# Performance work log

Hardware: AMD Instinct MI355X
Metric: run time of the kernel (lower is better)

Reference implementation:

```python
import jax, jax.numpy as jnp
import numpy as np


def _dense_image_warp(image, flow):
    """Faithful JAX port of tfa.image.dense_image_warp.

    image: [B,H,W,C] float, flow: [B,H,W,2] float (flow[...,0]=dy, flow[...,1]=dx).
    query point (y,x) = grid(y,x) - flow; bilinear interp with TFA's clamping:
    floor clipped to [0, size-2], alpha clipped to [0,1].
    """
    B, H, W, C = image.shape
    gy, gx = jnp.meshgrid(
        jnp.arange(H, dtype=flow.dtype), jnp.arange(W, dtype=flow.dtype), indexing="ij"
    )
    qy = gy[None] - flow[..., 0]  # [B,H,W]
    qx = gx[None] - flow[..., 1]

    y0f = jnp.clip(jnp.floor(qy), 0.0, H - 2)
    x0f = jnp.clip(jnp.floor(qx), 0.0, W - 2)
    ay = jnp.clip(qy - y0f, 0.0, 1.0)[..., None]  # [B,H,W,1]
    ax = jnp.clip(qx - x0f, 0.0, 1.0)[..., None]

    y0 = y0f.astype(jnp.int32)
    x0 = x0f.astype(jnp.int32)
    b = jnp.arange(B, dtype=jnp.int32)[:, None, None]

    tl = image[b, y0, x0]          # top-left  [B,H,W,C]
    tr = image[b, y0, x0 + 1]      # top-right
    bl = image[b, y0 + 1, x0]      # bottom-left
    br = image[b, y0 + 1, x0 + 1]  # bottom-right

    top = tl + ax * (tr - tl)
    bot = bl + ax * (br - bl)
    return top + ay * (bot - top)


def setup_inputs() -> dict:
    key = jax.random.key(0)
    k1, k2 = jax.random.split(key)
    B, H, W, C = 8, 1024, 768, 3
    image = jax.random.normal(k1, (B, H, W, C), dtype=jnp.float32)
    # flow magnitudes of a few pixels, typical for appearance-flow warping
    flow = jax.random.normal(k2, (B, H, W, 2), dtype=jnp.float32) * 5.0
    return {"image": image, "flow": flow}


def reference(image, flow):
    return _dense_image_warp(image, flow)
```

## Files before the change

kernel.cpp:

```cpp
#include <hip/hip_runtime.h>


constexpr int B = 8;
constexpr int H = 1024;
constexpr int W = 768;
constexpr int C = 3;

constexpr int TY = 32;
constexpr int TX = 24;
constexpr int TILES_Y = H / TY;
constexpr int COLS_X  = W / TX;

constexpr int WIN_COLS = 64;
constexpr int WSF = WIN_COLS * C;
constexpr int ROW_CHUNKS = WSF / 4;
constexpr int BAND = TY;
constexpr int RING_ROWS = 4 * BAND;
constexpr int BAND_GROUPS = BAND * ROW_CHUNKS / 64;
constexpr int NTHREADS = TY * TX;
constexpr int NWAVES = NTHREADS / 64;
constexpr int GPW = BAND_GROUPS / NWAVES;

static_assert(GPW * NWAVES == BAND_GROUPS, "uniform staging required for vmcnt");

typedef float vfloat2 __attribute__((ext_vector_type(2)));
typedef float vfloat4 __attribute__((ext_vector_type(4)));
typedef float vfloat2_a4 __attribute__((ext_vector_type(2), aligned(4)));
typedef float vfloat4_a4 __attribute__((ext_vector_type(4), aligned(4)));

__global__ __launch_bounds__(NTHREADS) void warp_kernel(
    const float* __restrict__ image,
    const float* __restrict__ flow,
    float* __restrict__ out)
{
    __shared__ float win[RING_ROWS * WSF];

    const int b  = blockIdx.x & 7;
    const int tx = blockIdx.x >> 3;
    const int X0 = tx * TX;
    const int colLo = min(max(X0 - 20, 0), W - WIN_COLS);

    const int lane = threadIdx.x & 63;
    const int wv   = threadIdx.x >> 6;

    const int py  = threadIdx.x / TX;
    const int pxx = threadIdx.x - py * TX;
    const int xg  = X0 + pxx;
    const float xgf = (float)xg;

    const float* gcol = image + (size_t)b * H * (W * C) + colLo * C;

    auto stage_band = [&](int k) {
        const int slotBase = (k & 3) * BAND;
#pragma unroll
        for (int i = 0; i < GPW; ++i) {
            const int j  = i * NWAVES + wv;
            const int ci = j * 64 + lane;
            const int r  = ci / ROW_CHUNKS;
            const int c  = ci - r * ROW_CHUNKS;
            const int rimg = min(k * BAND + r, H - 1);
            const float* g = gcol + (size_t)rimg * (W * C) + c * 4;
            __builtin_amdgcn_global_load_lds(
                (const __attribute__((address_space(1))) void*)g,
                (__attribute__((address_space(3))) void*)(win + slotBase * WSF + j * 256),
                16, 0, 0);
        }
    };

    auto load_flow = [&](int t) -> vfloat2 {
        const int yf = min(t * TY + py, H - 1);
        return __builtin_nontemporal_load(
            (const vfloat2*)flow + (((size_t)b * H + yf) * W + xg));
    };

    stage_band(0);
    stage_band(1);
    vfloat2 fcur = load_flow(0);

#pragma unroll 1
    for (int t = 0; t < TILES_Y; ++t) {
        stage_band(t + 2);
        const vfloat2 fnxt = load_flow(t + 1);

        asm volatile("s_waitcnt vmcnt(3)" ::: "memory");
        __builtin_amdgcn_s_barrier();
        __builtin_amdgcn_sched_barrier(0);

        const int Y0 = t * TY;
        const int y  = Y0 + py;

        const float qy = (float)y - fcur.x;
        const float qx = xgf      - fcur.y;

        float y0f = floorf(qy);
        float x0f = floorf(qx);
        y0f = fminf(fmaxf(y0f, 0.0f), (float)(H - 2));
        x0f = fminf(fmaxf(x0f, 0.0f), (float)(W - 2));
        const float ay = fminf(fmaxf(qy - y0f, 0.0f), 1.0f);
        const float ax = fminf(fmaxf(qx - x0f, 0.0f), 1.0f);
        const int y0 = (int)y0f;
        const int x0 = (int)x0f;

        float tl0, tl1, tl2, tr0, tr1, tr2, bl0, bl1, bl2, br0, br1, br2;

        const bool inwin = (y0 >= Y0 - BAND) & (y0 <= Y0 + 2 * BAND - 2) &
                           (x0 >= colLo) & (x0 <= colLo + WIN_COLS - 2);
        if (inwin) {
            const float* tp = &win[(y0 & (RING_ROWS - 1)) * WSF + (x0 - colLo) * C];
            const float* bp = &win[((y0 + 1) & (RING_ROWS - 1)) * WSF + (x0 - colLo) * C];
            tl0 = tp[0]; tl1 = tp[1]; tl2 = tp[2];
            tr0 = tp[3]; tr1 = tp[4]; tr2 = tp[5];
            bl0 = bp[0]; bl1 = bp[1]; bl2 = bp[2];
            br0 = bp[3]; br1 = bp[4]; br2 = bp[5];
        } else {
            const float* top = image + (((size_t)b * H + y0) * W + x0) * C;
            const float* bot = top + (size_t)W * C;
            const vfloat4 t4 = *(const vfloat4_a4*)top;
            const vfloat2 t2 = *(const vfloat2_a4*)(top + 4);
            const vfloat4 b4 = *(const vfloat4_a4*)bot;
            const vfloat2 b2 = *(const vfloat2_a4*)(bot + 4);
            tl0 = t4.x; tl1 = t4.y; tl2 = t4.z;
            tr0 = t4.w; tr1 = t2.x; tr2 = t2.y;
            bl0 = b4.x; bl1 = b4.y; bl2 = b4.z;
            br0 = b4.w; br1 = b2.x; br2 = b2.y;
        }

        const float tp0 = tl0 + ax * (tr0 - tl0);
        const float tp1 = tl1 + ax * (tr1 - tl1);
        const float tp2 = tl2 + ax * (tr2 - tl2);
        const float bo0 = bl0 + ax * (br0 - bl0);
        const float bo1 = bl1 + ax * (br1 - bl1);
        const float bo2 = bl2 + ax * (br2 - bl2);

        float* o = out + (((size_t)b * H + y) * W + xg) * C;
        __builtin_nontemporal_store(tp0 + ay * (bo0 - tp0), &o[0]);
        __builtin_nontemporal_store(tp1 + ay * (bo1 - tp1), &o[1]);
        __builtin_nontemporal_store(tp2 + ay * (bo2 - tp2), &o[2]);

        __builtin_amdgcn_s_barrier();
        __builtin_amdgcn_sched_barrier(0);
        fcur = fnxt;
    }
}

extern "C" void kernel_launch(void* const* d_in, const int* in_sizes, int n_in,
                              void* d_out, int out_size, void* d_ws, size_t ws_size,
                              hipStream_t stream) {
    const float* image = (const float*)d_in[0];
    const float* flow  = (const float*)d_in[1];
    float* out = (float*)d_out;

    dim3 grid(B * COLS_X);
    dim3 block(NTHREADS);
    warp_kernel<<<grid, block, 0, stream>>>(image, flow, out);
}
```

Baseline: 192.1 us.

## Sweep tiles along x with a panel ring buffer instead of along y

The kernel changes from blocks that own a column strip and walk down the rows to blocks that own a 16-row strip and walk across x in 32-pixel tiles. Each step stages a 49-row by 32-column panel into a four-slot LDS ring holding 128 columns. This cuts the per-block window footprint and makes flow loads and output stores contiguous along rows. The grid grows from 256 to 512 blocks of 512 threads with an occupancy hint of 4 blocks. The cost is a larger halo in y (49 rows staged for 16 output rows), which raises redundant image traffic through LDS, and a deeper vmcnt wait.

```diff
diff --git a/kernel.cpp b/kernel.cpp
--- a/kernel.cpp
+++ b/kernel.cpp
@@ -6,91 +6,94 @@
 constexpr int W = 768;
 constexpr int C = 3;
 
-constexpr int TY = 32;
-constexpr int TX = 24;
-constexpr int TILES_Y = H / TY;
-constexpr int COLS_X  = W / TX;
+constexpr int TY = 16, TX = 32;
+constexpr int TILES_X = W / TX;
+constexpr int STRIPS  = H / TY;
+constexpr int WIN_ROWS = 49;
+constexpr int ROW_CHUNKS = TX * C / 4;
+constexpr int PANEL_CHUNKS = WIN_ROWS * ROW_CHUNKS;
+constexpr int SLOT_FLOATS = PANEL_CHUNKS * 4;
+constexpr int LAST_BASE = PANEL_CHUNKS - 64;
 
-constexpr int WIN_COLS = 64;
-constexpr int WSF = WIN_COLS * C;
-constexpr int ROW_CHUNKS = WSF / 4;
-constexpr int BAND = TY;
-constexpr int RING_ROWS = 4 * BAND;
-constexpr int BAND_GROUPS = BAND * ROW_CHUNKS / 64;
 constexpr int NTHREADS = TY * TX;
 constexpr int NWAVES = NTHREADS / 64;
-constexpr int GPW = BAND_GROUPS / NWAVES;
-
-static_assert(GPW * NWAVES == BAND_GROUPS, "uniform staging required for vmcnt");
+constexpr int IPW = 3;
 
 typedef float vfloat2 __attribute__((ext_vector_type(2)));
 typedef float vfloat4 __attribute__((ext_vector_type(4)));
 typedef float vfloat2_a4 __attribute__((ext_vector_type(2), aligned(4)));
 typedef float vfloat4_a4 __attribute__((ext_vector_type(4), aligned(4)));
 
-__global__ __launch_bounds__(NTHREADS) void warp_kernel(
+__global__ __launch_bounds__(NTHREADS, 4) void warp_kernel(
     const float* __restrict__ image,
     const float* __restrict__ flow,
     float* __restrict__ out)
 {
-    __shared__ float win[RING_ROWS * WSF];
+    __shared__ float win[4 * SLOT_FLOATS];
 
     const int b  = blockIdx.x & 7;
-    const int tx = blockIdx.x >> 3;
-    const int X0 = tx * TX;
-    const int colLo = min(max(X0 - 20, 0), W - WIN_COLS);
+    const int gy = blockIdx.x >> 3;
+    const int Y0 = gy * TY;
+    const int rowLo = min(max(Y0 - 16, 0), H - WIN_ROWS);
 
     const int lane = threadIdx.x & 63;
     const int wv   = threadIdx.x >> 6;
 
-    const int py  = threadIdx.x / TX;
-    const int pxx = threadIdx.x - py * TX;
-    const int xg  = X0 + pxx;
-    const float xgf = (float)xg;
+    const int py  = threadIdx.x >> 5;
+    const int pxx = threadIdx.x & 31;
+    const int y   = Y0 + py;
+    const float yf = (float)y;
+    const size_t rowBase = ((size_t)b * H + y) * W;
 
-    const float* gcol = image + (size_t)b * H * (W * C) + colLo * C;
+    const float* gstrip = image + ((size_t)b * H + rowLo) * (W * C);
 
-    auto stage_band = [&](int k) {
-        const int slotBase = (k & 3) * BAND;
+    auto stage_panel = [&](int p) {
+        const int pe = min(max(p, 0), TILES_X - 1);
+        const float* gp = gstrip + pe * TX * C;
+        float* lp = win + (p & 3) * SLOT_FLOATS;
 #pragma unroll
-        for (int i = 0; i < GPW; ++i) {
-            const int j  = i * NWAVES + wv;
-            const int ci = j * 64 + lane;
-            const int r  = ci / ROW_CHUNKS;
-            const int c  = ci - r * ROW_CHUNKS;
-            const int rimg = min(k * BAND + r, H - 1);
-            const float* g = gcol + (size_t)rimg * (W * C) + c * 4;
+        for (int i = 0; i < IPW; ++i) {
+            const int j   = i * NWAVES + wv;
+            const int off = (j * 64 <= LAST_BASE) ? j * 64 : LAST_BASE;
+            const int ci  = off + lane;
+            const int r   = ci / ROW_CHUNKS;
+            const int c   = ci - r * ROW_CHUNKS;
+            const float* g = gp + (size_t)r * (W * C) + c * 4;
             __builtin_amdgcn_global_load_lds(
                 (const __attribute__((address_space(1))) void*)g,
-                (__attribute__((address_space(3))) void*)(win + slotBase * WSF + j * 256),
+                (__attribute__((address_space(3))) void*)(lp + off * 4),
                 16, 0, 0);
         }
     };
 
     auto load_flow = [&](int t) -> vfloat2 {
-        const int yf = min(t * TY + py, H - 1);
+        const int xe = min(t, TILES_X - 1) * TX + pxx;
         return __builtin_nontemporal_load(
-            (const vfloat2*)flow + (((size_t)b * H + yf) * W + xg));
+            (const vfloat2*)flow + (rowBase + xe));
     };
 
-    stage_band(0);
-    stage_band(1);
+    stage_panel(-1);
+    stage_panel(0);
+    stage_panel(1);
     vfloat2 fcur = load_flow(0);
+    asm volatile("s_waitcnt vmcnt(0)" ::: "memory");
+    __builtin_amdgcn_s_barrier();
+    __builtin_amdgcn_sched_barrier(0);
 
 #pragma unroll 1
-    for (int t = 0; t < TILES_Y; ++t) {
-        stage_band(t + 2);
+    for (int t = 0; t < TILES_X; ++t) {
+        stage_panel(t + 2);
         const vfloat2 fnxt = load_flow(t + 1);
 
-        asm volatile("s_waitcnt vmcnt(3)" ::: "memory");
+        asm volatile("s_waitcnt vmcnt(7)" ::: "memory");
         __builtin_amdgcn_s_barrier();
         __builtin_amdgcn_sched_barrier(0);
 
-        const int Y0 = t * TY;
-        const int y  = Y0 + py;
+        const int X0 = t * TX;
+        const int x  = X0 + pxx;
 
-        const float qy = (float)y - fcur.x;
-        const float qx = xgf      - fcur.y;
+        const float qy = yf        - fcur.x;
+        const float qx = (float)x  - fcur.y;
 
         float y0f = floorf(qy);
         float x0f = floorf(qx);
@@ -103,15 +106,19 @@
 
         float tl0, tl1, tl2, tr0, tr1, tr2, bl0, bl1, bl2, br0, br1, br2;
 
-        const bool inwin = (y0 >= Y0 - BAND) & (y0 <= Y0 + 2 * BAND - 2) &
-                           (x0 >= colLo) & (x0 <= colLo + WIN_COLS - 2);
+        const bool inwin = (y0 >= rowLo) & (y0 <= rowLo + WIN_ROWS - 2) &
+                           (x0 >= X0 - 16) & (x0 <= X0 + 46);
         if (inwin) {
-            const float* tp = &win[(y0 & (RING_ROWS - 1)) * WSF + (x0 - colLo) * C];
-            const float* bp = &win[((y0 + 1) & (RING_ROWS - 1)) * WSF + (x0 - colLo) * C];
-            tl0 = tp[0]; tl1 = tp[1]; tl2 = tp[2];
-            tr0 = tp[3]; tr1 = tp[4]; tr2 = tp[5];
-            bl0 = bp[0]; bl1 = bp[1]; bl2 = bp[2];
-            br0 = bp[3]; br1 = bp[4]; br2 = bp[5];
+            const int ry = y0 - rowLo;
+            const int x1 = x0 + 1;
+            const float* aL = win + ((x0 >> 5) & 3) * SLOT_FLOATS
+                                  + ry * (TX * C) + (x0 & 31) * C;
+            const float* aR = win + ((x1 >> 5) & 3) * SLOT_FLOATS
+                                  + ry * (TX * C) + (x1 & 31) * C;
+            tl0 = aL[0]; tl1 = aL[1]; tl2 = aL[2];
+            bl0 = aL[TX * C + 0]; bl1 = aL[TX * C + 1]; bl2 = aL[TX * C + 2];
+            tr0 = aR[0]; tr1 = aR[1]; tr2 = aR[2];
+            br0 = aR[TX * C + 0]; br1 = aR[TX * C + 1]; br2 = aR[TX * C + 2];
         } else {
             const float* top = image + (((size_t)b * H + y0) * W + x0) * C;
             const float* bot = top + (size_t)W * C;
@@ -132,7 +139,7 @@
         const float bo1 = bl1 + ax * (br1 - bl1);
         const float bo2 = bl2 + ax * (br2 - bl2);
 
-        float* o = out + (((size_t)b * H + y) * W + xg) * C;
+        float* o = out + (rowBase + x) * C;
         __builtin_nontemporal_store(tp0 + ay * (bo0 - tp0), &o[0]);
         __builtin_nontemporal_store(tp1 + ay * (bo1 - tp1), &o[1]);
         __builtin_nontemporal_store(tp2 + ay * (bo2 - tp2), &o[2]);
@@ -150,7 +157,7 @@
     const float* flow  = (const float*)d_in[1];
     float* out = (float*)d_out;
 
-    dim3 grid(B * COLS_X);
+    dim3 grid(B * STRIPS);
     dim3 block(NTHREADS);
     warp_kernel<<<grid, block, 0, stream>>>(image, flow, out);
 }
```

Measured after the change: 179.5 us. -6.5%, faster.
